# Kernel optimization log

Hardware: AMD Instinct MI355X
Metric: run time of the kernel (lower is better)

## Reference

```python
import jax, jax.numpy as jnp
import numpy as np

MINING_MARGIN = 0.1
MARGIN = 0.3
EPS = 1e-6  # torch F.pairwise_distance adds eps to the elementwise difference


def _normalize(v):
    # torch F.normalize(p=2): v / max(||v||, 1e-12)
    n = jnp.linalg.norm(v, axis=-1, keepdims=True)
    return v / jnp.maximum(n, 1e-12)


def setup_inputs() -> dict:
    key = jax.random.key(0)
    x = jax.random.normal(key, (16384, 2, 256), dtype=jnp.float32)
    return {"x": x}


def reference(x):
    a = _normalize(x[:, 0, :])  # [B, D] anchors
    p = _normalize(x[:, 1, :])  # [B, D] positives
    # mining uses detached embeddings
    ad = jax.lax.stop_gradient(a)
    pd = jax.lax.stop_gradient(p)
    B, d = ad.shape

    # Full pairwise distance matrix D[i, j] = ||ad[i] - pd[j] + EPS||_2,
    # expanded algebraically to avoid a [B, B, D] intermediate:
    # ||a - p + e||^2 = ||a||^2 + ||p||^2 - 2 a.p + 2e*(sum(a) - sum(p)) + d*e^2
    dot = ad @ pd.T                                   # [B, B]
    na2 = jnp.sum(ad * ad, axis=1)                    # [B]
    np2 = jnp.sum(pd * pd, axis=1)                    # [B]
    sa = jnp.sum(ad, axis=1)                          # [B]
    sp = jnp.sum(pd, axis=1)                          # [B]
    D2 = (na2[:, None] + np2[None, :] - 2.0 * dot
          + 2.0 * EPS * (sa[:, None] - sp[None, :]) + d * EPS * EPS)
    D = jnp.sqrt(jnp.clip(D2, 0.0))                   # [B, B]

    diag = jnp.diagonal(D)                            # anchor-to-own-positive dist
    # semihard: farther than positive but within mining_margin
    mask = (D > diag[:, None]) & (D < diag[:, None] + MINING_MARGIN)

    # GPU-side uniform random choice per row among masked candidates
    k1, k2 = jax.random.split(jax.random.key(1))
    g = jax.random.uniform(k1, (B, B))
    scores = jnp.where(mask, g, -1.0)
    cand = jnp.argmax(scores, axis=1)                 # random masked index
    fallback = jax.random.randint(k2, (B,), 0, B)     # random.choice(posidx)
    negidx = jnp.where(jnp.any(mask, axis=1), cand, fallback)

    neg = p[negidx]                                   # [B, D]
    pos_dist = jnp.linalg.norm(a - p + EPS, axis=1)
    neg_dist = jnp.linalg.norm(a - neg + EPS, axis=1)
    loss = jnp.mean(jax.nn.relu(pos_dist ** 2 - neg_dist ** 2 + MARGIN))
    return loss
```

## Files before the change

### kernel.cpp

```cpp
#include <hip/hip_runtime.h>
#include <stdint.h>

#define B_N 16384
#define DIMV 256
#define XSTRIDE 512
#define EPSF 1e-6f
#define CEF 2.56e-10f
#define TWOEPS 2e-6f
#define MINING 0.1f
#define MARGINF 0.3f
#define NSTRIP 8

typedef __attribute__((ext_vector_type(8))) short bf16x8;
typedef __attribute__((ext_vector_type(4))) float f32x4;

__device__ __forceinline__ void tf2x32(uint32_t k0, uint32_t k1,
                                       uint32_t& x0, uint32_t& x1) {
  uint32_t k2 = k0 ^ k1 ^ 0x1BD11BDAu;
  x0 += k0; x1 += k1;
#define TFR(r) { x0 += x1; x1 = (x1 << (r)) | (x1 >> (32 - (r))); x1 ^= x0; }
  TFR(13) TFR(15) TFR(26) TFR(6)
  x0 += k1; x1 += k2 + 1u;
  TFR(17) TFR(29) TFR(16) TFR(24)
  x0 += k2; x1 += k0 + 2u;
  TFR(13) TFR(15) TFR(26) TFR(6)
  x0 += k0; x1 += k1 + 3u;
  TFR(17) TFR(29) TFR(16) TFR(24)
  x0 += k1; x1 += k2 + 4u;
  TFR(13) TFR(15) TFR(26) TFR(6)
  x0 += k2; x1 += k0 + 5u;
#undef TFR
}

#define TF_ROT(x, r) __builtin_amdgcn_alignbit((x), (x), 32u - (r))

__device__ __forceinline__ uint32_t tf_mb(uint32_t K0, uint32_t K1, uint32_t c1) {
  const uint32_t K2 = K0 ^ K1 ^ 0x1BD11BDAu;
  uint32_t x0 = K0;
  uint32_t x1 = c1 + K1;
#define R4A { x0 += x1; x1 = TF_ROT(x1, 13); x1 ^= x0; \
              x0 += x1; x1 = TF_ROT(x1, 15); x1 ^= x0; \
              x0 += x1; x1 = TF_ROT(x1, 26); x1 ^= x0; \
              x0 += x1; x1 = TF_ROT(x1, 6);  x1 ^= x0; }
#define R4B { x0 += x1; x1 = TF_ROT(x1, 17); x1 ^= x0; \
              x0 += x1; x1 = TF_ROT(x1, 29); x1 ^= x0; \
              x0 += x1; x1 = TF_ROT(x1, 16); x1 ^= x0; \
              x0 += x1; x1 = TF_ROT(x1, 24); x1 ^= x0; }
  R4A; x0 += K1; x1 += K2 + 1u;
  R4B; x0 += K2; x1 += K0 + 2u;
  R4A; x0 += K0; x1 += K1 + 3u;
  R4B; x0 += K1; x1 += K2 + 4u;
  R4A; x0 += K2; x1 += K0 + 5u;
#undef R4A
#undef R4B
  return (x0 ^ x1) >> 9;
}

__device__ __forceinline__ float wave_sum(float v) {
#pragma unroll
  for (int off = 32; off > 0; off >>= 1) v += __shfl_xor(v, off, 64);
  return v;
}

__device__ __forceinline__ void gl_lds16(const unsigned short* g, unsigned short* s) {
  __builtin_amdgcn_global_load_lds(
      (const __attribute__((address_space(1))) void*)g,
      (__attribute__((address_space(3))) void*)s, 16, 0, 0);
}

__device__ __forceinline__ uint32_t split_pack(float v) {
  const uint32_t u = __float_as_uint(v);
  const uint32_t hi = (u + 0x7FFFu + ((u >> 16) & 1u)) >> 16;
  const float hf = __uint_as_float(hi << 16);
  const float lf = v - hf;
  const uint32_t ul = __float_as_uint(lf);
  const uint32_t lo = (ul + 0x7FFFu + ((ul >> 16) & 1u)) >> 16;
  return hi | (lo << 16);
}

__global__ void k1_stats(const float* __restrict__ x, float* __restrict__ invA,
                         float* __restrict__ invP, float* __restrict__ rowA,
                         float* __restrict__ colB, float* __restrict__ lo,
                         float* __restrict__ pos2) {
  const int i = blockIdx.x;
  const int l = threadIdx.x;
  const float4 va = *(const float4*)&x[i * XSTRIDE + l * 4];
  const float4 vp = *(const float4*)&x[i * XSTRIDE + DIMV + l * 4];
  float saa = va.x*va.x + va.y*va.y + va.z*va.z + va.w*va.w;
  float spp = vp.x*vp.x + vp.y*vp.y + vp.z*vp.z + vp.w*vp.w;
  saa = wave_sum(saa); spp = wave_sum(spp);
  const float ia = 1.0f / fmaxf(sqrtf(saa), 1e-12f);
  const float ip = 1.0f / fmaxf(sqrtf(spp), 1e-12f);
  const float ax = va.x*ia, ay = va.y*ia, az = va.z*ia, aw = va.w*ia;
  const float px = vp.x*ip, py = vp.y*ip, pz = vp.z*ip, pw = vp.w*ip;
  float na2 = ax*ax + ay*ay + az*az + aw*aw;
  float np2 = px*px + py*py + pz*pz + pw*pw;
  float sa  = ax + ay + az + aw;
  float sp  = px + py + pz + pw;
  float dii = ax*px + ay*py + az*pz + aw*pw;
  const float dx = ax-px+EPSF, dy = ay-py+EPSF, dz = az-pz+EPSF, dw = aw-pw+EPSF;
  float ps = dx*dx + dy*dy + dz*dz + dw*dw;
  na2 = wave_sum(na2); np2 = wave_sum(np2); sa = wave_sum(sa);
  sp  = wave_sum(sp);  dii = wave_sum(dii); ps = wave_sum(ps);
  if (l == 0) {
    const float rA = na2 + TWOEPS * sa + CEF;
    const float cB = np2 - TWOEPS * sp;
    invA[i] = ia; invP[i] = ip; rowA[i] = rA; colB[i] = cB;
    lo[i] = sqrtf(fmaxf(rA + cB - 2.0f * dii, 0.0f));
    pos2[i] = ps;
  }
}

__global__ void k1b_cvt(const float* __restrict__ x, const float* __restrict__ invA,
                        const float* __restrict__ invP,
                        unsigned short* __restrict__ Abf,
                        unsigned short* __restrict__ Pbf) {
  const int t = blockIdx.x * 256 + threadIdx.x;
  const int row = t >> 6, l = t & 63;
  const float ia = invA[row], ip = invP[row];
  const float4 va = *(const float4*)&x[row * XSTRIDE + l * 4];
  const float4 vp = *(const float4*)&x[row * XSTRIDE + DIMV + l * 4];
  uint4 oa, op;
  oa.x = split_pack(va.x * ia); oa.y = split_pack(va.y * ia);
  oa.z = split_pack(va.z * ia); oa.w = split_pack(va.w * ia);
  op.x = split_pack(vp.x * ip); op.y = split_pack(vp.y * ip);
  op.z = split_pack(vp.z * ip); op.w = split_pack(vp.w * ip);
  *(uint4*)&Abf[(size_t)row * 512 + l * 8] = oa;
  *(uint4*)&Pbf[(size_t)row * 512 + l * 8] = op;
}

__global__ __launch_bounds__(256, 2) void k2_mfma_bm(
    const unsigned short* __restrict__ Abf, const unsigned short* __restrict__ Pbf,
    const float* __restrict__ rowA, const float* __restrict__ colB,
    const float* __restrict__ lo, unsigned long long* __restrict__ bitmap) {
  __shared__ __align__(16) unsigned short As[64 * 64];
  __shared__ __align__(16) unsigned short Bs[128 * 64];

  const int tid = threadIdx.x;
  const int w = tid >> 6;
  const int l = tid & 63;
  const int q = l >> 4;
  const int c16 = l & 15;
  const int rBase = blockIdx.x * 64;
  const int strip = blockIdx.y;

  const int sw = c16 & 7;
  const int sgk = (l & 7) ^ ((l >> 3) & 7);

  const int arow = rBase + w * 16 + (l >> 3);
  const unsigned short* gA0 = Abf + (size_t)arow * 512 + sgk * 8;
  unsigned short* lA0 = &As[(w * 16) * 64];
  unsigned short* lB0 = &Bs[(w * 32) * 64];

  unsigned long long* wordsBlk =
      bitmap + ((size_t)blockIdx.x * NSTRIP + strip) * 2048;

  float Lr[4], Hr[4];
  const int iBase = rBase + w * 16 + q * 4;
#pragma unroll
  for (int ri = 0; ri < 4; ++ri) {
    const int i = iBase + ri;
    const float ra = rowA[i];
    const float lv = lo[i];
    Lr[ri] = lv * lv - ra;
    Hr[ri] = (lv + MINING) * (lv + MINING) - ra;
  }

  for (int ct = 0; ct < 16; ++ct) {
    const int cBase = strip * 2048 + ct * 128;
    const int brow = cBase + w * 32 + (l >> 3);
    const unsigned short* gB0 = Pbf + (size_t)brow * 512 + sgk * 8;

    f32x4 acc[8];
#pragma unroll
    for (int n = 0; n < 8; ++n) {
      f32x4 z = {0.0f, 0.0f, 0.0f, 0.0f};
      acc[n] = z;
    }

    for (int kc = 0; kc < 512; kc += 64) {
      __syncthreads();
#pragma unroll
      for (int u = 0; u < 2; ++u)
        gl_lds16(gA0 + kc + u * 8 * 512, lA0 + u * 8 * 64);
#pragma unroll
      for (int u = 0; u < 4; ++u)
        gl_lds16(gB0 + kc + u * 8 * 512, lB0 + u * 8 * 64);
      __syncthreads();
#pragma unroll
      for (int ks = 0; ks < 2; ++ks) {
        const int px = ((ks * 4 + q) ^ sw) * 8;
        const bf16x8 am = *(const bf16x8*)&As[(w * 16 + c16) * 64 + px];
        bf16x8 bn[8];
#pragma unroll
        for (int n = 0; n < 8; ++n)
          bn[n] = *(const bf16x8*)&Bs[(n * 16 + c16) * 64 + px];
#pragma unroll
        for (int n = 0; n < 8; ++n)
          acc[n] = __builtin_amdgcn_mfma_f32_16x16x32_bf16(am, bn[n], acc[n],
                                                           0, 0, 0);
      }
    }

#pragma unroll
    for (int n = 0; n < 8; ++n) {
      const int j = cBase + n * 16 + c16;
      const float cb = colB[j];
#pragma unroll
      for (int ri = 0; ri < 4; ++ri) {
        const int i = iBase + ri;
        const float t = fmaf(-2.0f, acc[n][ri], cb);
        const bool pred = (t > Lr[ri]) & (t < Hr[ri]) & (j != i);
        const unsigned long long bal = __ballot(pred);
        if (l == 0)
          wordsBlk[((w * 16 + ct) * 8 + n) * 4 + ri] = bal;
      }
    }
  }
}

__global__ __launch_bounds__(256, 4) void k3b_draw(
    const unsigned long long* __restrict__ bitmap,
    unsigned long long* __restrict__ partials) {
  __shared__ unsigned long long slots[64];
  const int tid = threadIdx.x;
  const int rt = blockIdx.x, strip = blockIdx.y;
  if (tid < 64) slots[tid] = 0ull;
  __syncthreads();

  uint32_t K0 = 0u, K1 = 0u;
  tf2x32(0u, 1u, K0, K1);

  const unsigned long long* wordsBlk =
      bitmap + ((size_t)rt * NSTRIP + strip) * 2048;
  const int rowBase = rt * 64;
  const int colBase = strip * 2048;

  unsigned long long bits = 0ull;
  int wiCur = 0;
  int wiNext = tid;
  for (;;) {
    while (bits == 0ull && wiNext < 2048) {
      bits = wordsBlk[wiNext];
      wiCur = wiNext;
      wiNext += 256;
    }
    if (bits == 0ull) break;
    const int b = __ffsll(bits) - 1;
    bits &= bits - 1ull;
    const int ri = wiCur & 3;
    const int n  = (wiCur >> 2) & 7;
    const int ct = (wiCur >> 5) & 15;
    const int w  = wiCur >> 9;
    const int i = rowBase + w * 16 + (b >> 4) * 4 + ri;
    const int j = colBase + ct * 128 + n * 16 + (b & 15);
    const uint32_t mb = tf_mb(K0, K1, ((uint32_t)i << 14) | (uint32_t)j);
    const unsigned long long key =
        ((unsigned long long)(mb + 1u) << 32) |
        (unsigned long long)(uint32_t)(16383 - j);
    atomicMax(&slots[i & 63], key);
  }
  __syncthreads();
  if (tid < 64)
    partials[(size_t)(rowBase + tid) * NSTRIP + strip] = slots[tid];
}

__global__ __launch_bounds__(256, 2) void k2_mfma_dense(
    const unsigned short* __restrict__ Abf, const unsigned short* __restrict__ Pbf,
    const float* __restrict__ rowA, const float* __restrict__ colB,
    const float* __restrict__ lo, unsigned long long* __restrict__ partials) {
  __shared__ __align__(16) unsigned short As[64 * 64];
  __shared__ __align__(16) unsigned short Bs[128 * 64];

  const int tid = threadIdx.x;
  const int w = tid >> 6;
  const int l = tid & 63;
  const int q = l >> 4;
  const int c16 = l & 15;
  const int rBase = blockIdx.x * 64;
  const int strip = blockIdx.y;

  uint32_t K0 = 0u, K1 = 0u;
  tf2x32(0u, 1u, K0, K1);

  const int sw = c16 & 7;
  const int sgk = (l & 7) ^ ((l >> 3) & 7);

  const int arow = rBase + w * 16 + (l >> 3);
  const unsigned short* gA0 = Abf + (size_t)arow * 512 + sgk * 8;
  unsigned short* lA0 = &As[(w * 16) * 64];
  unsigned short* lB0 = &Bs[(w * 32) * 64];

  float Lr[4], Hr[4];
  const int iBase = rBase + w * 16 + q * 4;
#pragma unroll
  for (int ri = 0; ri < 4; ++ri) {
    const int i = iBase + ri;
    const float ra = rowA[i];
    const float lv = lo[i];
    Lr[ri] = lv * lv - ra;
    Hr[ri] = (lv + MINING) * (lv + MINING) - ra;
  }

  int bmb[4], bj[4];
#pragma unroll
  for (int ri = 0; ri < 4; ++ri) { bmb[ri] = -1; bj[ri] = 0; }

  for (int ct = 0; ct < 16; ++ct) {
    const int cBase = strip * 2048 + ct * 128;
    const int brow = cBase + w * 32 + (l >> 3);
    const unsigned short* gB0 = Pbf + (size_t)brow * 512 + sgk * 8;

    f32x4 acc[8];
#pragma unroll
    for (int n = 0; n < 8; ++n) {
      f32x4 z = {0.0f, 0.0f, 0.0f, 0.0f};
      acc[n] = z;
    }

    for (int kc = 0; kc < 512; kc += 64) {
      __syncthreads();
#pragma unroll
      for (int u = 0; u < 2; ++u)
        gl_lds16(gA0 + kc + u * 8 * 512, lA0 + u * 8 * 64);
#pragma unroll
      for (int u = 0; u < 4; ++u)
        gl_lds16(gB0 + kc + u * 8 * 512, lB0 + u * 8 * 64);
      __syncthreads();
#pragma unroll
      for (int ks = 0; ks < 2; ++ks) {
        const int px = ((ks * 4 + q) ^ sw) * 8;
        const bf16x8 am = *(const bf16x8*)&As[(w * 16 + c16) * 64 + px];
        bf16x8 bn[8];
#pragma unroll
        for (int n = 0; n < 8; ++n)
          bn[n] = *(const bf16x8*)&Bs[(n * 16 + c16) * 64 + px];
#pragma unroll
        for (int n = 0; n < 8; ++n)
          acc[n] = __builtin_amdgcn_mfma_f32_16x16x32_bf16(am, bn[n], acc[n],
                                                           0, 0, 0);
      }
    }

#pragma unroll
    for (int n = 0; n < 8; ++n) {
      const int j = cBase + n * 16 + c16;
      const float cb = colB[j];
#pragma unroll
      for (int ri = 0; ri < 4; ++ri) {
        const int i = iBase + ri;
        const float t = fmaf(-2.0f, acc[n][ri], cb);
        const uint32_t mb = tf_mb(K0, K1, ((uint32_t)i << 14) | (uint32_t)j);
        const bool upd = (t > Lr[ri]) & (t < Hr[ri]) & (j != i) &
                         ((int)mb > bmb[ri]);
        bmb[ri] = upd ? (int)mb : bmb[ri];
        bj[ri]  = upd ? j : bj[ri];
      }
    }
  }

#pragma unroll
  for (int ri = 0; ri < 4; ++ri) {
    unsigned long long bk = 0ull;
    if (bmb[ri] >= 0)
      bk = ((unsigned long long)(uint32_t)(bmb[ri] + 1) << 32) |
           (unsigned long long)(uint32_t)(16383 - bj[ri]);
#pragma unroll
    for (int off = 1; off < 16; off <<= 1) {
      const unsigned long long o = __shfl_xor(bk, off, 64);
      if (o > bk) bk = o;
    }
    if (c16 == 0)
      partials[(size_t)(iBase + ri) * NSTRIP + strip] = bk;
  }
}

#define TM 64
#define TN 128
#define KC 64
#define AS_LD 68
#define BS_LD 132
#define COLS_PER_STRIP (B_N / NSTRIP)
#define TILES_PER_STRIP (COLS_PER_STRIP / TN)

__global__ __launch_bounds__(256, 3) void k2_mine(
    const float* __restrict__ x, const float* __restrict__ invA,
    const float* __restrict__ invP, const float* __restrict__ rowA,
    const float* __restrict__ colB, const float* __restrict__ lo,
    unsigned long long* __restrict__ partials) {
  __shared__ __align__(16) float As[KC * AS_LD];
  __shared__ __align__(16) float Bs[KC * BS_LD];
  __shared__ float colBs[TN];

  const int tid = threadIdx.x;
  const int ty = tid >> 4;
  const int tx = tid & 15;
  const int rBase = blockIdx.x * TM;
  const int strip = blockIdx.y;
  const int cStart = strip * COLS_PER_STRIP;

  uint32_t k1h = 0u, k1l = 0u;
  tf2x32(0u, 1u, k1h, k1l);

  float rowA_r[4], lo_r[4];
  int rows[4];
#pragma unroll
  for (int m = 0; m < 4; ++m) {
    rows[m] = rBase + ty * 4 + m;
    rowA_r[m] = rowA[rows[m]];
    lo_r[m] = lo[rows[m]];
  }

  unsigned long long best[4] = {0ull, 0ull, 0ull, 0ull};
  const int skq = tid & 15;
  const int srr = tid >> 4;

  for (int ct = 0; ct < TILES_PER_STRIP; ++ct) {
    const int cBase = cStart + ct * TN;
    float acc[4][8];
#pragma unroll
    for (int m = 0; m < 4; ++m)
#pragma unroll
      for (int n = 0; n < 8; ++n) acc[m][n] = 0.0f;

    for (int kc = 0; kc < DIMV; kc += KC) {
      __syncthreads();
#pragma unroll
      for (int u = 0; u < 4; ++u) {
        const int r = srr + 16 * u;
        const int row = rBase + r;
        const float4 v = *(const float4*)&x[row * XSTRIDE + kc + skq * 4];
        const float s = invA[row];
        As[(skq * 4 + 0) * AS_LD + r] = v.x * s;
        As[(skq * 4 + 1) * AS_LD + r] = v.y * s;
        As[(skq * 4 + 2) * AS_LD + r] = v.z * s;
        As[(skq * 4 + 3) * AS_LD + r] = v.w * s;
      }
#pragma unroll
      for (int u = 0; u < 8; ++u) {
        const int c = srr + 16 * u;
        const int col = cBase + c;
        const float4 v = *(const float4*)&x[col * XSTRIDE + DIMV + kc + skq * 4];
        const float s = invP[col];
        Bs[(skq * 4 + 0) * BS_LD + c] = v.x * s;
        Bs[(skq * 4 + 1) * BS_LD + c] = v.y * s;
        Bs[(skq * 4 + 2) * BS_LD + c] = v.z * s;
        Bs[(skq * 4 + 3) * BS_LD + c] = v.w * s;
      }
      if (kc == 0 && tid < TN) colBs[tid] = colB[cBase + tid];
      __syncthreads();

#pragma unroll 8
      for (int k = 0; k < KC; ++k) {
        const float4 a4 = *(const float4*)&As[k * AS_LD + ty * 4];
        const float4 bl = *(const float4*)&Bs[k * BS_LD + tx * 4];
        const float4 bh = *(const float4*)&Bs[k * BS_LD + 64 + tx * 4];
        const float am[4] = {a4.x, a4.y, a4.z, a4.w};
        const float bn[8] = {bl.x, bl.y, bl.z, bl.w, bh.x, bh.y, bh.z, bh.w};
#pragma unroll
        for (int m = 0; m < 4; ++m)
#pragma unroll
          for (int n = 0; n < 8; ++n)
            acc[m][n] = fmaf(am[m], bn[n], acc[m][n]);
      }
    }

#pragma unroll
    for (int m = 0; m < 4; ++m) {
      const int i = rows[m];
      const float loi = lo_r[m];
      const float hii = loi + MINING;
#pragma unroll
      for (int n = 0; n < 8; ++n) {
        const int cOff = (n < 4) ? (tx * 4 + n) : (64 + tx * 4 + (n - 4));
        const int j = cBase + cOff;
        const float D2 = rowA_r[m] + colBs[cOff] - 2.0f * acc[m][n];
        const float D = sqrtf(fmaxf(D2, 0.0f));
        if (D > loi && D < hii && j != i) {
          uint32_t c0 = 0u;
          uint32_t c1 = ((uint32_t)i << 14) | (uint32_t)j;
          tf2x32(k1h, k1l, c0, c1);
          const uint32_t bits = c0 ^ c1;
          const uint32_t mb = bits >> 9;
          const unsigned long long pk =
              ((unsigned long long)(mb + 1u) << 32) |
              (unsigned long long)(uint32_t)(16383 - j);
          if (pk > best[m]) best[m] = pk;
        }
      }
    }
  }

  __syncthreads();
  unsigned long long* red = (unsigned long long*)As;
#pragma unroll
  for (int m = 0; m < 4; ++m) red[(ty * 4 + m) * 16 + tx] = best[m];
  __syncthreads();
  if (tid < TM) {
    unsigned long long g = red[tid * 16];
#pragma unroll
    for (int t = 1; t < 16; ++t) {
      const unsigned long long v = red[tid * 16 + t];
      if (v > g) g = v;
    }
    partials[(size_t)(rBase + tid) * NSTRIP + strip] = g;
  }
}

__global__ void k3_select(const unsigned long long* __restrict__ partials,
                          int* __restrict__ negidx) {
  const int i = blockIdx.x * 256 + threadIdx.x;
  unsigned long long g = 0ull;
#pragma unroll
  for (int s = 0; s < NSTRIP; ++s) {
    const unsigned long long v = partials[(size_t)i * NSTRIP + s];
    if (v > g) g = v;
  }
  int ng;
  if (g != 0ull) {
    ng = 16383 - (int)(g & 0xFFFFFFFFull);
  } else {
    uint32_t t0 = 0u, t1 = 1u;
    tf2x32(0u, 1u, t0, t1);
    uint32_t u0 = 0u, u1 = 1u;
    tf2x32(t0, t1, u0, u1);
    uint32_t v0 = 0u, v1 = (uint32_t)i;
    tf2x32(u0, u1, v0, v1);
    ng = (int)((v0 ^ v1) & 16383u);
  }
  negidx[i] = ng;
}

__global__ void k4_loss(const float* __restrict__ x, const float* __restrict__ invA,
                        const float* __restrict__ invP, const float* __restrict__ pos2,
                        const int* __restrict__ negidx, float* __restrict__ bsums) {
  const int w = threadIdx.x >> 6;
  const int l = threadIdx.x & 63;
  const int i = blockIdx.x * 4 + w;
  const float ia = invA[i];
  const int ng = negidx[i];
  const float ip = invP[ng];
  const float4 va = *(const float4*)&x[i * XSTRIDE + l * 4];
  const float4 vn = *(const float4*)&x[ng * XSTRIDE + DIMV + l * 4];
  const float dx = va.x * ia - vn.x * ip + EPSF;
  const float dy = va.y * ia - vn.y * ip + EPSF;
  const float dz = va.z * ia - vn.z * ip + EPSF;
  const float dw = va.w * ia - vn.w * ip + EPSF;
  float s = dx*dx + dy*dy + dz*dz + dw*dw;
  s = wave_sum(s);
  __shared__ float bs[4];
  if (l == 0) bs[w] = fmaxf(pos2[i] - s + MARGINF, 0.0f);
  __syncthreads();
  if (threadIdx.x == 0) bsums[blockIdx.x] = bs[0] + bs[1] + bs[2] + bs[3];
}

__global__ void k5_reduce(const float* __restrict__ bsums, float* __restrict__ out) {
  float s = 0.0f;
  for (int idx = threadIdx.x; idx < (B_N / 4); idx += 256) s += bsums[idx];
  s = wave_sum(s);
  __shared__ float acc4[4];
  if ((threadIdx.x & 63) == 0) acc4[threadIdx.x >> 6] = s;
  __syncthreads();
  if (threadIdx.x == 0)
    out[0] = (acc4[0] + acc4[1] + acc4[2] + acc4[3]) * (1.0f / (float)B_N);
}

extern "C" void kernel_launch(void* const* d_in, const int* in_sizes, int n_in,
                              void* d_out, int out_size, void* d_ws, size_t ws_size,
                              hipStream_t stream) {
  const float* x = (const float*)d_in[0];
  char* ws = (char*)d_ws;
  size_t off = 0;
  unsigned long long* partials = (unsigned long long*)(ws + off);
  off += (size_t)B_N * NSTRIP * sizeof(unsigned long long);
  float* invA = (float*)(ws + off); off += (size_t)B_N * 4;
  float* invP = (float*)(ws + off); off += (size_t)B_N * 4;
  float* rowA = (float*)(ws + off); off += (size_t)B_N * 4;
  float* colB = (float*)(ws + off); off += (size_t)B_N * 4;
  float* lo   = (float*)(ws + off); off += (size_t)B_N * 4;
  float* pos2 = (float*)(ws + off); off += (size_t)B_N * 4;
  int* negidx = (int*)(ws + off);   off += (size_t)B_N * 4;
  float* bsums = (float*)(ws + off); off += (size_t)(B_N / 4) * 4;
  unsigned short* Abf = (unsigned short*)(ws + off);
  off += (size_t)B_N * 512 * sizeof(unsigned short);
  unsigned short* Pbf = (unsigned short*)(ws + off);
  off += (size_t)B_N * 512 * sizeof(unsigned short);
  const size_t ws_need_bf16 = off;
  unsigned long long* bitmap = (unsigned long long*)(ws + off);
  off += (size_t)2048 * 2048 * sizeof(unsigned long long);
  const size_t ws_need_bitmap = off;
  float* out = (float*)d_out;

  hipLaunchKernelGGL(k1_stats, dim3(B_N), dim3(64), 0, stream,
                     x, invA, invP, rowA, colB, lo, pos2);
  if (ws_size >= ws_need_bitmap) {
    hipLaunchKernelGGL(k1b_cvt, dim3(B_N / 4), dim3(256), 0, stream,
                       x, invA, invP, Abf, Pbf);
    hipLaunchKernelGGL(k2_mfma_bm, dim3(B_N / 64, NSTRIP), dim3(256), 0, stream,
                       Abf, Pbf, rowA, colB, lo, bitmap);
    hipLaunchKernelGGL(k3b_draw, dim3(B_N / 64, NSTRIP), dim3(256), 0, stream,
                       bitmap, partials);
  } else if (ws_size >= ws_need_bf16) {
    hipLaunchKernelGGL(k1b_cvt, dim3(B_N / 4), dim3(256), 0, stream,
                       x, invA, invP, Abf, Pbf);
    hipLaunchKernelGGL(k2_mfma_dense, dim3(B_N / 64, NSTRIP), dim3(256), 0,
                       stream, Abf, Pbf, rowA, colB, lo, partials);
  } else {
    hipLaunchKernelGGL(k2_mine, dim3(B_N / TM, NSTRIP), dim3(256), 0, stream,
                       x, invA, invP, rowA, colB, lo, partials);
  }
  hipLaunchKernelGGL(k3_select, dim3(B_N / 256), dim3(256), 0, stream,
                     partials, negidx);
  hipLaunchKernelGGL(k4_loss, dim3(B_N / 4), dim3(256), 0, stream,
                     x, invA, invP, pos2, negidx, bsums);
  hipLaunchKernelGGL(k5_reduce, dim3(1), dim3(256), 0, stream, bsums, out);
}
```

Baseline: 960.1 us.

## Replace sparse bitmap draw with dense per-lane threefry scan and shuffle reduction

The draw kernel used to walk only the set bits of the semihard bitmap, computing a threefry random for each candidate and resolving winners with LDS atomicMax. It now has each lane own a fixed (row, column) position, compute threefry for every one of its 512 positions, keep a per-row running max in registers, and reduce across 16 lanes with shuffles. This removes LDS atomics, the data-dependent while loop and the divergence that comes with it, at the cost of hashing every pair whether masked or not. That cost grows with total pairs instead of with mask density.

```diff
diff --git a/kernel.cpp b/kernel.cpp
--- a/kernel.cpp
+++ b/kernel.cpp
@@ -219,50 +219,63 @@
   }
 }
 
-__global__ __launch_bounds__(256, 4) void k3b_draw(
+__global__ __launch_bounds__(256, 8) void k3c_draw(
     const unsigned long long* __restrict__ bitmap,
     unsigned long long* __restrict__ partials) {
-  __shared__ unsigned long long slots[64];
   const int tid = threadIdx.x;
   const int rt = blockIdx.x, strip = blockIdx.y;
-  if (tid < 64) slots[tid] = 0ull;
-  __syncthreads();
+  const int l = tid & 63;
+  const int q = l >> 4;
+  const int c16 = l & 15;
+  const int w = __builtin_amdgcn_readfirstlane(tid >> 6);
 
   uint32_t K0 = 0u, K1 = 0u;
   tf2x32(0u, 1u, K0, K1);
 
-  const unsigned long long* wordsBlk =
-      bitmap + ((size_t)rt * NSTRIP + strip) * 2048;
-  const int rowBase = rt * 64;
+  const unsigned long long* wordsW =
+      bitmap + ((size_t)rt * NSTRIP + strip) * 2048 + (size_t)w * 512;
+  const unsigned long long lmask = 1ull << l;
+
+  int bmb[4] = {-1, -1, -1, -1};
+  int bj[4]  = {0, 0, 0, 0};
+
   const int colBase = strip * 2048;
-
-  unsigned long long bits = 0ull;
-  int wiCur = 0;
-  int wiNext = tid;
-  for (;;) {
-    while (bits == 0ull && wiNext < 2048) {
-      bits = wordsBlk[wiNext];
-      wiCur = wiNext;
-      wiNext += 256;
-    }
-    if (bits == 0ull) break;
-    const int b = __ffsll(bits) - 1;
-    bits &= bits - 1ull;
-    const int ri = wiCur & 3;
-    const int n  = (wiCur >> 2) & 7;
-    const int ct = (wiCur >> 5) & 15;
-    const int w  = wiCur >> 9;
-    const int i = rowBase + w * 16 + (b >> 4) * 4 + ri;
-    const int j = colBase + ct * 128 + n * 16 + (b & 15);
-    const uint32_t mb = tf_mb(K0, K1, ((uint32_t)i << 14) | (uint32_t)j);
-    const unsigned long long key =
-        ((unsigned long long)(mb + 1u) << 32) |
-        (unsigned long long)(uint32_t)(16383 - j);
-    atomicMax(&slots[i & 63], key);
-  }
-  __syncthreads();
-  if (tid < 64)
-    partials[(size_t)(rowBase + tid) * NSTRIP + strip] = slots[tid];
+  const uint32_t ib = ((uint32_t)(rt * 64 + w * 16 + q * 4)) << 14;
+
+  for (int ct = 0; ct < 16; ++ct) {
+    const int jct = colBase + ct * 128;
+#pragma unroll
+    for (int n = 0; n < 8; ++n) {
+      const int j = jct + n * 16 + c16;
+      const uint32_t cb = ib + (uint32_t)j;
+      unsigned long long wv[4];
+#pragma unroll
+      for (int ri = 0; ri < 4; ++ri)
+        wv[ri] = wordsW[ct * 32 + n * 4 + ri];
+#pragma unroll
+      for (int ri = 0; ri < 4; ++ri) {
+        const uint32_t mb = tf_mb(K0, K1, cb + ((uint32_t)ri << 14));
+        const bool upd = ((wv[ri] & lmask) != 0ull) & ((int)mb > bmb[ri]);
+        bmb[ri] = upd ? (int)mb : bmb[ri];
+        bj[ri]  = upd ? j : bj[ri];
+      }
+    }
+  }
+
+#pragma unroll
+  for (int ri = 0; ri < 4; ++ri) {
+    unsigned long long bk = 0ull;
+    if (bmb[ri] >= 0)
+      bk = ((unsigned long long)(uint32_t)(bmb[ri] + 1) << 32) |
+           (unsigned long long)(uint32_t)(16383 - bj[ri]);
+#pragma unroll
+    for (int off = 1; off < 16; off <<= 1) {
+      const unsigned long long o = __shfl_xor(bk, off, 64);
+      if (o > bk) bk = o;
+    }
+    if (c16 == 0)
+      partials[(size_t)(rt * 64 + w * 16 + q * 4 + ri) * NSTRIP + strip] = bk;
+  }
 }
 
 __global__ __launch_bounds__(256, 2) void k2_mfma_dense(
@@ -598,7 +611,7 @@
                        x, invA, invP, Abf, Pbf);
     hipLaunchKernelGGL(k2_mfma_bm, dim3(B_N / 64, NSTRIP), dim3(256), 0, stream,
                        Abf, Pbf, rowA, colB, lo, bitmap);
-    hipLaunchKernelGGL(k3b_draw, dim3(B_N / 64, NSTRIP), dim3(256), 0, stream,
+    hipLaunchKernelGGL(k3c_draw, dim3(B_N / 64, NSTRIP), dim3(256), 0, stream,
                        bitmap, partials);
   } else if (ws_size >= ws_need_bf16) {
     hipLaunchKernelGGL(k1b_cvt, dim3(B_N / 4), dim3(256), 0, stream,
```

Measured after the change: 1.041 ms. 1.08x slower.
